# Kernel optimization log

Measured on AMD Instinct MI355X. Metric: run time of the kernel, lower is better.

The kernel has to match this reference:

```python
import jax, jax.numpy as jnp
import numpy as np

HEADS = 4
DIM_HEAD = 128


def setup_inputs() -> dict:
    key = jax.random.key(0)
    k1, k2, k3, k4 = jax.random.split(key, 4)
    B, C, H, W = 8, 256, 64, 64
    hidden = HEADS * DIM_HEAD  # 512
    x = jax.random.normal(k1, (B, C, H, W), dtype=jnp.float32)
    # 1x1 convs are just channel matmuls; store kernels as [out_ch, in_ch]
    w_qkv = jax.random.normal(k2, (3 * hidden, C), dtype=jnp.float32) * 0.05
    w_out = jax.random.normal(k3, (C, hidden), dtype=jnp.float32) * 0.05
    b_out = jax.random.normal(k4, (C,), dtype=jnp.float32) * 0.05
    return {"x": x, "w_qkv": w_qkv, "w_out": w_out, "b_out": b_out}


def reference(x, w_qkv, w_out, b_out):
    B, C, H, W = x.shape
    n = H * W
    # to_qkv: 1x1 conv without bias == channel matmul
    qkv = jnp.einsum('bchw,oc->bohw', x, w_qkv)  # [B, 3*heads*dim_head, H, W]
    qkv = qkv.reshape(B, 3, HEADS, DIM_HEAD, n)  # 'b (qkv heads c) h w -> b qkv heads c n'
    q, k, v = qkv[:, 0], qkv[:, 1], qkv[:, 2]    # each [B, heads, dim_head, n]
    k = jax.nn.softmax(k, axis=-1)               # softmax over spatial positions
    context = jnp.einsum('bhdn,bhen->bhde', k, v)   # [B, heads, d, e]
    out = jnp.einsum('bhde,bhdn->bhen', context, q)  # [B, heads, e, n]
    out = out.reshape(B, HEADS * DIM_HEAD, H, W)
    # to_out: 1x1 conv with bias
    return jnp.einsum('bchw,oc->bohw', out, w_out) + b_out[None, :, None, None]
```

## Files before the change

kernel.cpp:

```cpp
#include <hip/hip_runtime.h>
#include <stdint.h>


using frag8 = __attribute__((ext_vector_type(8))) short;
using f32x4 = __attribute__((ext_vector_type(4))) float;

__device__ __forceinline__ float bf2f(unsigned short u) {
    union { unsigned int u; float f; } c;
    c.u = ((unsigned int)u) << 16;
    return c.f;
}
__device__ __forceinline__ unsigned short f2bf(float f) {
    union { float f; unsigned int u; } c; c.f = f;
    unsigned int u = c.u;
    return (unsigned short)((u + 0x7FFFu + ((u >> 16) & 1u)) >> 16);
}

__device__ __forceinline__ void gl_lds16(const void* g, void* l) {
    __builtin_amdgcn_global_load_lds(
        (const __attribute__((address_space(1))) unsigned int*)g,
        (__attribute__((address_space(3))) unsigned int*)l, 16, 0, 0);
}

__global__ __launch_bounds__(256) void k0_weights(
    const float* __restrict__ w_qkv, const float* __restrict__ w_out,
    unsigned short* __restrict__ wkb, unsigned short* __restrict__ wqT,
    unsigned short* __restrict__ U, float* __restrict__ rs)
{
    __shared__ float T[64][65];
    const int blk = blockIdx.x;
    const int tid = threadIdx.x;
    if (blk < 128) {
        const int idx = (blk * 256 + tid) * 4;
        float4 v = *(const float4*)(w_qkv + 512 * 256 + idx);
        ushort4 o;
        o.x = f2bf(v.x); o.y = f2bf(v.y); o.z = f2bf(v.z); o.w = f2bf(v.w);
        *(ushort4*)(wkb + idx) = o;
    } else if (blk < 160) {
        const int t = blk - 128;
        const int j0 = (t >> 2) * 64, c0 = (t & 3) * 64;
        const int r = tid >> 4, cc = (tid & 15) * 4;
        #pragma unroll
        for (int p = 0; p < 4; ++p) {
            float4 v = *(const float4*)(w_qkv + (j0 + r + p * 16) * 256 + c0 + cc);
            T[r + p * 16][cc + 0] = v.x; T[r + p * 16][cc + 1] = v.y;
            T[r + p * 16][cc + 2] = v.z; T[r + p * 16][cc + 3] = v.w;
        }
        __syncthreads();
        const int c = tid >> 2, jj = (tid & 3) * 16;
        #pragma unroll
        for (int g = 0; g < 4; ++g) {
            ushort4 o;
            o.x = f2bf(T[jj + g * 4 + 0][c]);
            o.y = f2bf(T[jj + g * 4 + 1][c]);
            o.z = f2bf(T[jj + g * 4 + 2][c]);
            o.w = f2bf(T[jj + g * 4 + 3][c]);
            *(ushort4*)(wqT + (c0 + c) * 512 + j0 + jj + g * 4) = o;
        }
    } else if (blk < 224) {
        float (*As)[65] = &T[0];
        float (*Bs)[65] = &T[16];
        const int ub = blk - 160;
        const int h = ub >> 4, rem = ub & 15;
        const int o0 = (rem >> 2) * 64, c0 = (rem & 3) * 64;
        const int tm = tid >> 4, tn = tid & 15;
        const int ar = tid >> 2, ac = (tid & 3) * 4;
        const int br = tid >> 4, bc = (tid & 15) * 4;
        float acc[4][4] = {};
        for (int e0 = 0; e0 < 128; e0 += 16) {
            float4 a4 = *(const float4*)(w_out + (o0 + ar) * 512 + h * 128 + e0 + ac);
            float4 b4 = *(const float4*)(w_qkv + (1024 + h * 128 + e0 + br) * 256 + c0 + bc);
            __syncthreads();
            As[ac + 0][ar] = a4.x; As[ac + 1][ar] = a4.y;
            As[ac + 2][ar] = a4.z; As[ac + 3][ar] = a4.w;
            Bs[br][bc + 0] = b4.x; Bs[br][bc + 1] = b4.y;
            Bs[br][bc + 2] = b4.z; Bs[br][bc + 3] = b4.w;
            __syncthreads();
            #pragma unroll
            for (int kk = 0; kk < 16; ++kk) {
                float a[4], bb[4];
                #pragma unroll
                for (int i = 0; i < 4; ++i) a[i] = As[kk][tm * 4 + i];
                #pragma unroll
                for (int j = 0; j < 4; ++j) bb[j] = Bs[kk][tn * 4 + j];
                #pragma unroll
                for (int i = 0; i < 4; ++i)
                    #pragma unroll
                    for (int j = 0; j < 4; ++j) acc[i][j] += a[i] * bb[j];
            }
        }
        #pragma unroll
        for (int i = 0; i < 4; ++i) {
            ushort4 o;
            o.x = f2bf(acc[i][0]); o.y = f2bf(acc[i][1]);
            o.z = f2bf(acc[i][2]); o.w = f2bf(acc[i][3]);
            *(ushort4*)(U + h * 65536 + (o0 + tm * 4 + i) * 256 + c0 + tn * 4) = o;
        }
    } else {
        const int idx = ((blk - 224) * 256 + tid) * 4;
        *(float4*)(rs + idx) = make_float4(0.f, 0.f, 0.f, 0.f);
    }
}

__global__ __launch_bounds__(256) void k0_xt(
    const float* __restrict__ x, unsigned short* __restrict__ xbT,
    unsigned short* __restrict__ xbc)
{
    __shared__ float T[64][65];
    const int tid = threadIdx.x;
    const int n0 = blockIdx.x * 64, c0 = blockIdx.y * 64, b = blockIdx.z;
    const float* xb = x + (size_t)b * 1048576;
    const int cr = tid >> 4, nc = (tid & 15) * 4;
    #pragma unroll
    for (int p = 0; p < 4; ++p) {
        float4 v = *(const float4*)(xb + (size_t)(c0 + cr + p * 16) * 4096 + n0 + nc);
        T[cr + p * 16][nc + 0] = v.x; T[cr + p * 16][nc + 1] = v.y;
        T[cr + p * 16][nc + 2] = v.z; T[cr + p * 16][nc + 3] = v.w;
        ushort4 o;
        o.x = f2bf(v.x); o.y = f2bf(v.y); o.z = f2bf(v.z); o.w = f2bf(v.w);
        *(ushort4*)(xbc + (size_t)b * 1048576 + (size_t)(c0 + cr + p * 16) * 4096 + n0 + nc) = o;
    }
    __syncthreads();
    const int n = tid >> 2, cc = (tid & 3) * 16;
    unsigned short* dst = xbT + (size_t)b * 1048576 + (size_t)(n0 + n) * 256 + c0 + cc;
    #pragma unroll
    for (int g = 0; g < 4; ++g) {
        ushort4 o;
        o.x = f2bf(T[cc + g * 4 + 0][n]);
        o.y = f2bf(T[cc + g * 4 + 1][n]);
        o.z = f2bf(T[cc + g * 4 + 2][n]);
        o.w = f2bf(T[cc + g * 4 + 3][n]);
        *(ushort4*)(dst + g * 4) = o;
    }
}

template<int MODE>
__global__ __launch_bounds__(256) void mfma_bt(
    const unsigned short* __restrict__ A0, int lda,
    const unsigned short* __restrict__ B0, int ldb,
    void* __restrict__ C0, int ldc,
    const float* __restrict__ bias, int Kp,
    unsigned long long sAz, unsigned long long sBz, unsigned long long sCz,
    float* __restrict__ aux)
{
    __shared__ unsigned short As[128 * 32];
    __shared__ unsigned short Bs[128 * 32];
    const int tid  = threadIdx.x;
    const int w    = tid >> 6, lane = tid & 63;
    const int quad = lane >> 4, l16 = lane & 15;
    const int wm = (w >> 1) * 64, wn = (w & 1) * 64;
    const int z = blockIdx.z;

    const unsigned short* A;
    const unsigned short* B;
    int ks, ke, m0, n0;
    if constexpr (MODE == 3) {
        m0 = blockIdx.y * 128; n0 = 0;
        ks = 0; ke = 256;
        A = A0 + (unsigned long long)(z & 3) * 65536ull + (unsigned long long)m0 * lda;
        B = B0 + (unsigned long long)(z >> 2) * 131072ull + (unsigned long long)(z & 3) * 32768ull;
    } else if constexpr (MODE == 4) {
        m0 = blockIdx.y * 128; n0 = (blockIdx.x & 1) * 128;
        ks = (blockIdx.x >> 1) * 1024; ke = ks + 1024;
        A = A0 + sAz * z + (unsigned long long)m0 * lda;
        B = B0 + sBz * z + (unsigned long long)n0 * ldb;
    } else {
        m0 = blockIdx.y * 128; n0 = blockIdx.x * 128;
        ks = 0; ke = Kp;
        A = A0 + sAz * z + (unsigned long long)m0 * lda;
        B = B0 + sBz * z + (unsigned long long)n0 * ldb;
    }

    const int cA0 = w * 128 + lane;
    const int cA1 = cA0 + 64;
    const unsigned short* gA0 = A + (unsigned long long)(cA0 >> 2) * lda + (cA0 & 3) * 8;
    const unsigned short* gA1 = A + (unsigned long long)(cA1 >> 2) * lda + (cA1 & 3) * 8;
    const unsigned short* gB0 = B + (unsigned long long)(cA0 >> 2) * ldb + (cA0 & 3) * 8;
    const unsigned short* gB1 = B + (unsigned long long)(cA1 >> 2) * ldb + (cA1 & 3) * 8;
    unsigned short* lA0 = As + w * 1024;
    unsigned short* lA1 = As + w * 1024 + 512;
    unsigned short* lB0 = Bs + w * 1024;
    unsigned short* lB1 = Bs + w * 1024 + 512;

    f32x4 acc[4][4] = {};

    for (int k0 = ks; k0 < ke; k0 += 32) {
        gl_lds16(gA0 + k0, lA0);
        gl_lds16(gA1 + k0, lA1);
        gl_lds16(gB0 + k0, lB0);
        gl_lds16(gB1 + k0, lB1);
        __syncthreads();
        frag8 a[4], b[4];
        #pragma unroll
        for (int t = 0; t < 4; ++t) {
            a[t] = *(const frag8*)(As + (wm + t * 16 + l16) * 32 + quad * 8);
            b[t] = *(const frag8*)(Bs + (wn + t * 16 + l16) * 32 + quad * 8);
        }
        #pragma unroll
        for (int mt = 0; mt < 4; ++mt)
            #pragma unroll
            for (int nt = 0; nt < 4; ++nt)
                acc[mt][nt] = __builtin_amdgcn_mfma_f32_16x16x32_bf16(
                    a[mt], b[nt], acc[mt][nt], 0, 0, 0);
        __syncthreads();
    }

    if constexpr (MODE == 0 || MODE == 3) {
        unsigned short* C;
        if constexpr (MODE == 0)
            C = (unsigned short*)C0 + sCz * z + (unsigned long long)m0 * ldc + n0;
        else
            C = (unsigned short*)C0 + (unsigned long long)(z >> 2) * 131072ull
              + (unsigned long long)(z & 3) * 128ull + (unsigned long long)m0 * ldc;
        #pragma unroll
        for (int mt = 0; mt < 4; ++mt) {
            const int row = wm + mt * 16 + quad * 4;
            #pragma unroll
            for (int nt = 0; nt < 4; ++nt) {
                const int col = wn + nt * 16 + l16;
                #pragma unroll
                for (int r = 0; r < 4; ++r)
                    C[(unsigned long long)(row + r) * ldc + col] = f2bf(acc[mt][nt][r]);
            }
        }
    } else if constexpr (MODE == 1) {
        float* C = (float*)C0 + sCz * z + (unsigned long long)m0 * ldc + n0;
        const float* bp = bias + m0;
        #pragma unroll
        for (int mt = 0; mt < 4; ++mt) {
            const int row = wm + mt * 16 + quad * 4;
            #pragma unroll
            for (int nt = 0; nt < 4; ++nt) {
                const int col = wn + nt * 16 + l16;
                #pragma unroll
                for (int r = 0; r < 4; ++r)
                    C[(unsigned long long)(row + r) * ldc + col] = acc[mt][nt][r] + bp[row + r];
            }
        }
    } else if constexpr (MODE == 4) {
        float* C = (float*)C0 + (unsigned long long)(blockIdx.x >> 1) * 1048576ull
                 + sCz * z + (unsigned long long)m0 * ldc + n0;
        #pragma unroll
        for (int mt = 0; mt < 4; ++mt) {
            const int row = wm + mt * 16 + quad * 4;
            #pragma unroll
            for (int nt = 0; nt < 4; ++nt) {
                const int col = wn + nt * 16 + l16;
                #pragma unroll
                for (int r = 0; r < 4; ++r)
                    C[(unsigned long long)(row + r) * ldc + col] = acc[mt][nt][r];
            }
        }
    } else {
        unsigned short* C = (unsigned short*)C0 + sCz * z
                          + (unsigned long long)m0 * ldc + n0;
        float rp[4][4] = {};
        #pragma unroll
        for (int mt = 0; mt < 4; ++mt) {
            const int row = wm + mt * 16 + quad * 4;
            #pragma unroll
            for (int nt = 0; nt < 4; ++nt) {
                const int col = wn + nt * 16 + l16;
                #pragma unroll
                for (int r = 0; r < 4; ++r) {
                    const float e = __expf(acc[mt][nt][r]);
                    C[(unsigned long long)(row + r) * ldc + col] = f2bf(e);
                    rp[mt][r] += e;
                }
            }
        }
        #pragma unroll
        for (int m = 1; m < 16; m <<= 1)
            #pragma unroll
            for (int mt = 0; mt < 4; ++mt)
                #pragma unroll
                for (int r = 0; r < 4; ++r)
                    rp[mt][r] += __shfl_xor(rp[mt][r], m, 64);
        if (l16 == 0) {
            float* rsb = aux + z * 512 + m0;
            #pragma unroll
            for (int mt = 0; mt < 4; ++mt)
                #pragma unroll
                for (int r = 0; r < 4; ++r)
                    atomicAdd(rsb + wm + mt * 16 + quad * 4 + r, rp[mt][r]);
        }
    }
}

__global__ __launch_bounds__(256) void k3_sum(
    const float* __restrict__ Gp, const float* __restrict__ rs,
    unsigned short* __restrict__ G)
{
    const int idx = (blockIdx.x * 256 + threadIdx.x) * 4;
    const float inv = 1.0f / rs[idx >> 8];
    float4 s = make_float4(0.f, 0.f, 0.f, 0.f);
    #pragma unroll
    for (int sl = 0; sl < 4; ++sl) {
        float4 t = *(const float4*)(Gp + (size_t)sl * 1048576 + idx);
        s.x += t.x; s.y += t.y; s.z += t.z; s.w += t.w;
    }
    ushort4 o;
    o.x = f2bf(s.x * inv); o.y = f2bf(s.y * inv);
    o.z = f2bf(s.z * inv); o.w = f2bf(s.w * inv);
    *(ushort4*)(G + idx) = o;
}

extern "C" void kernel_launch(void* const* d_in, const int* in_sizes, int n_in,
                              void* d_out, int out_size, void* d_ws, size_t ws_size,
                              hipStream_t stream) {
    (void)in_sizes; (void)n_in; (void)out_size; (void)ws_size;
    const float* x     = (const float*)d_in[0];
    const float* w_qkv = (const float*)d_in[1];
    const float* w_out = (const float*)d_in[2];
    const float* b_out = (const float*)d_in[3];
    float* out = (float*)d_out;

    char* ws = (char*)d_ws;
    unsigned short* Kexp = (unsigned short*)ws;
    unsigned short* xbT  = (unsigned short*)(ws + 33554432);
    unsigned short* xbc  = (unsigned short*)(ws + 50331648);
    unsigned short* wkb  = (unsigned short*)(ws + 67108864);
    unsigned short* wqT  = (unsigned short*)(ws + 67371008);
    unsigned short* U    = (unsigned short*)(ws + 67633152);
    float*          rs   = (float*)(ws + 68157440);
    float*          Gp   = (float*)(ws + 68173824);
    unsigned short* G    = (unsigned short*)(ws + 84951040);
    unsigned short* Mb   = (unsigned short*)(ws + 87048192);
    unsigned short* Nb   = (unsigned short*)(ws + 89145344);

    k0_weights<<<dim3(228), 256, 0, stream>>>(w_qkv, w_out, wkb, wqT, U, rs);
    k0_xt<<<dim3(64, 4, 8), 256, 0, stream>>>(x, xbT, xbc);
    mfma_bt<5><<<dim3(32, 4, 8), 256, 0, stream>>>(
        wkb, 256, xbT, 256, Kexp, 4096, nullptr, 256,
        0ull, 1048576ull, 2097152ull, rs);
    mfma_bt<4><<<dim3(8, 4, 8), 256, 0, stream>>>(
        Kexp, 4096, xbc, 4096, Gp, 256, nullptr, 0,
        2097152ull, 1048576ull, 131072ull, nullptr);
    k3_sum<<<dim3(1024), 256, 0, stream>>>(Gp, rs, G);
    mfma_bt<3><<<dim3(1, 2, 32), 256, 0, stream>>>(
        U, 256, G, 256, Mb, 512, nullptr, 256,
        0ull, 0ull, 0ull, nullptr);
    mfma_bt<0><<<dim3(2, 2, 8), 256, 0, stream>>>(
        Mb, 512, wqT, 512, Nb, 256, nullptr, 512,
        131072ull, 0ull, 65536ull, nullptr);
    mfma_bt<1><<<dim3(32, 2, 8), 256, 0, stream>>>(
        Nb, 256, xbT, 256, out, 4096, b_out, 256,
        65536ull, 1048576ull, 1048576ull, nullptr);
}
```

Baseline: 201.5 us.

## Merge prep kernels, widen GEMM K-step, stage epilogue through LDS

```diff
diff --git a/kernel.cpp b/kernel.cpp
--- a/kernel.cpp
+++ b/kernel.cpp
@@ -4,6 +4,7 @@
 
 using frag8 = __attribute__((ext_vector_type(8))) short;
 using f32x4 = __attribute__((ext_vector_type(4))) float;
+typedef unsigned short us8 __attribute__((ext_vector_type(8)));
 
 __device__ __forceinline__ float bf2f(unsigned short u) {
     union { unsigned int u; float f; } c;
@@ -22,115 +23,126 @@
         (__attribute__((address_space(3))) unsigned int*)l, 16, 0, 0);
 }
 
-__global__ __launch_bounds__(256) void k0_weights(
-    const float* __restrict__ w_qkv, const float* __restrict__ w_out,
+__global__ __launch_bounds__(256) void k0_all(
+    const float* __restrict__ x, const float* __restrict__ w_qkv,
+    const float* __restrict__ w_out,
+    unsigned short* __restrict__ xbT, unsigned short* __restrict__ xbc,
     unsigned short* __restrict__ wkb, unsigned short* __restrict__ wqT,
     unsigned short* __restrict__ U, float* __restrict__ rs)
 {
-    __shared__ float T[64][65];
+    __shared__ __align__(16) unsigned char sm[68096];
     const int blk = blockIdx.x;
     const int tid = threadIdx.x;
-    if (blk < 128) {
-        const int idx = (blk * 256 + tid) * 4;
-        float4 v = *(const float4*)(w_qkv + 512 * 256 + idx);
-        ushort4 o;
-        o.x = f2bf(v.x); o.y = f2bf(v.y); o.z = f2bf(v.z); o.w = f2bf(v.w);
-        *(ushort4*)(wkb + idx) = o;
-    } else if (blk < 160) {
-        const int t = blk - 128;
-        const int j0 = (t >> 2) * 64, c0 = (t & 3) * 64;
-        const int r = tid >> 4, cc = (tid & 15) * 4;
-        #pragma unroll
-        for (int p = 0; p < 4; ++p) {
-            float4 v = *(const float4*)(w_qkv + (j0 + r + p * 16) * 256 + c0 + cc);
-            T[r + p * 16][cc + 0] = v.x; T[r + p * 16][cc + 1] = v.y;
-            T[r + p * 16][cc + 2] = v.z; T[r + p * 16][cc + 3] = v.w;
+    if (blk < 512) {
+        float (*T)[133] = (float(*)[133])sm;
+        const int b = blk >> 6, rem = blk & 63;
+        const int n0 = (rem >> 1) * 128, c0 = (rem & 1) * 128;
+        const float* xb = x + (size_t)b * 1048576;
+        const int rr = tid >> 5, cc4 = (tid & 31) * 4;
+        #pragma unroll
+        for (int p = 0; p < 16; ++p) {
+            const int r = rr + p * 8;
+            float4 v = *(const float4*)(xb + (size_t)(c0 + r) * 4096 + n0 + cc4);
+            T[r][cc4 + 0] = v.x; T[r][cc4 + 1] = v.y;
+            T[r][cc4 + 2] = v.z; T[r][cc4 + 3] = v.w;
         }
         __syncthreads();
-        const int c = tid >> 2, jj = (tid & 3) * 16;
-        #pragma unroll
-        for (int g = 0; g < 4; ++g) {
+        const int nr = tid >> 4, c8 = (tid & 15) * 8;
+        unsigned short* dst = xbT + (size_t)b * 1048576 + (size_t)n0 * 256 + c0;
+        #pragma unroll
+        for (int p = 0; p < 8; ++p) {
+            const int n = nr + p * 16;
+            us8 o;
+            #pragma unroll
+            for (int j = 0; j < 8; ++j) o[j] = f2bf(T[c8 + j][n]);
+            *(us8*)(dst + (size_t)n * 256 + c8) = o;
+        }
+    } else if (blk < 1024) {
+        const int base = (blk - 512) * 16384;
+        #pragma unroll
+        for (int p = 0; p < 8; ++p) {
+            const int idx = base + p * 2048 + tid * 8;
+            float4 a = *(const float4*)(x + idx);
+            float4 b = *(const float4*)(x + idx + 4);
+            us8 o;
+            o[0] = f2bf(a.x); o[1] = f2bf(a.y); o[2] = f2bf(a.z); o[3] = f2bf(a.w);
+            o[4] = f2bf(b.x); o[5] = f2bf(b.y); o[6] = f2bf(b.z); o[7] = f2bf(b.w);
+            *(us8*)(xbc + idx) = o;
+        }
+    } else {
+        const int wb = blk - 1024;
+        if (wb < 128) {
+            const int idx = (wb * 256 + tid) * 4;
+            float4 v = *(const float4*)(w_qkv + 512 * 256 + idx);
             ushort4 o;
-            o.x = f2bf(T[jj + g * 4 + 0][c]);
-            o.y = f2bf(T[jj + g * 4 + 1][c]);
-            o.z = f2bf(T[jj + g * 4 + 2][c]);
-            o.w = f2bf(T[jj + g * 4 + 3][c]);
-            *(ushort4*)(wqT + (c0 + c) * 512 + j0 + jj + g * 4) = o;
-        }
-    } else if (blk < 224) {
-        float (*As)[65] = &T[0];
-        float (*Bs)[65] = &T[16];
-        const int ub = blk - 160;
-        const int h = ub >> 4, rem = ub & 15;
-        const int o0 = (rem >> 2) * 64, c0 = (rem & 3) * 64;
-        const int tm = tid >> 4, tn = tid & 15;
-        const int ar = tid >> 2, ac = (tid & 3) * 4;
-        const int br = tid >> 4, bc = (tid & 15) * 4;
-        float acc[4][4] = {};
-        for (int e0 = 0; e0 < 128; e0 += 16) {
-            float4 a4 = *(const float4*)(w_out + (o0 + ar) * 512 + h * 128 + e0 + ac);
-            float4 b4 = *(const float4*)(w_qkv + (1024 + h * 128 + e0 + br) * 256 + c0 + bc);
+            o.x = f2bf(v.x); o.y = f2bf(v.y); o.z = f2bf(v.z); o.w = f2bf(v.w);
+            *(ushort4*)(wkb + idx) = o;
+        } else if (wb < 160) {
+            float (*T)[65] = (float(*)[65])sm;
+            const int t = wb - 128;
+            const int j0 = (t >> 2) * 64, c0 = (t & 3) * 64;
+            const int r = tid >> 4, cc = (tid & 15) * 4;
+            #pragma unroll
+            for (int p = 0; p < 4; ++p) {
+                float4 v = *(const float4*)(w_qkv + (j0 + r + p * 16) * 256 + c0 + cc);
+                T[r + p * 16][cc + 0] = v.x; T[r + p * 16][cc + 1] = v.y;
+                T[r + p * 16][cc + 2] = v.z; T[r + p * 16][cc + 3] = v.w;
+            }
             __syncthreads();
-            As[ac + 0][ar] = a4.x; As[ac + 1][ar] = a4.y;
-            As[ac + 2][ar] = a4.z; As[ac + 3][ar] = a4.w;
-            Bs[br][bc + 0] = b4.x; Bs[br][bc + 1] = b4.y;
-            Bs[br][bc + 2] = b4.z; Bs[br][bc + 3] = b4.w;
-            __syncthreads();
-            #pragma unroll
-            for (int kk = 0; kk < 16; ++kk) {
-                float a[4], bb[4];
-                #pragma unroll
-                for (int i = 0; i < 4; ++i) a[i] = As[kk][tm * 4 + i];
-                #pragma unroll
-                for (int j = 0; j < 4; ++j) bb[j] = Bs[kk][tn * 4 + j];
-                #pragma unroll
-                for (int i = 0; i < 4; ++i)
+            const int c = tid >> 2, jj = (tid & 3) * 16;
+            #pragma unroll
+            for (int g = 0; g < 4; ++g) {
+                ushort4 o;
+                o.x = f2bf(T[jj + g * 4 + 0][c]);
+                o.y = f2bf(T[jj + g * 4 + 1][c]);
+                o.z = f2bf(T[jj + g * 4 + 2][c]);
+                o.w = f2bf(T[jj + g * 4 + 3][c]);
+                *(ushort4*)(wqT + (c0 + c) * 512 + j0 + jj + g * 4) = o;
+            }
+        } else if (wb < 224) {
+            float (*T)[65] = (float(*)[65])sm;
+            float (*As)[65] = &T[0];
+            float (*Bs)[65] = &T[16];
+            const int ub = wb - 160;
+            const int h = ub >> 4, rem = ub & 15;
+            const int o0 = (rem >> 2) * 64, c0 = (rem & 3) * 64;
+            const int tm = tid >> 4, tn = tid & 15;
+            const int ar = tid >> 2, ac = (tid & 3) * 4;
+            const int br = tid >> 4, bc = (tid & 15) * 4;
+            float acc[4][4] = {};
+            for (int e0 = 0; e0 < 128; e0 += 16) {
+                float4 a4 = *(const float4*)(w_out + (o0 + ar) * 512 + h * 128 + e0 + ac);
+                float4 b4 = *(const float4*)(w_qkv + (1024 + h * 128 + e0 + br) * 256 + c0 + bc);
+                __syncthreads();
+                As[ac + 0][ar] = a4.x; As[ac + 1][ar] = a4.y;
+                As[ac + 2][ar] = a4.z; As[ac + 3][ar] = a4.w;
+                Bs[br][bc + 0] = b4.x; Bs[br][bc + 1] = b4.y;
+                Bs[br][bc + 2] = b4.z; Bs[br][bc + 3] = b4.w;
+                __syncthreads();
+                #pragma unroll
+                for (int kk = 0; kk < 16; ++kk) {
+                    float a[4], bb[4];
                     #pragma unroll
-                    for (int j = 0; j < 4; ++j) acc[i][j] += a[i] * bb[j];
-            }
-        }
-        #pragma unroll
-        for (int i = 0; i < 4; ++i) {
-            ushort4 o;
-            o.x = f2bf(acc[i][0]); o.y = f2bf(acc[i][1]);
-            o.z = f2bf(acc[i][2]); o.w = f2bf(acc[i][3]);
-            *(ushort4*)(U + h * 65536 + (o0 + tm * 4 + i) * 256 + c0 + tn * 4) = o;
-        }
-    } else {
-        const int idx = ((blk - 224) * 256 + tid) * 4;
-        *(float4*)(rs + idx) = make_float4(0.f, 0.f, 0.f, 0.f);
-    }
-}
-
-__global__ __launch_bounds__(256) void k0_xt(
-    const float* __restrict__ x, unsigned short* __restrict__ xbT,
-    unsigned short* __restrict__ xbc)
-{
-    __shared__ float T[64][65];
-    const int tid = threadIdx.x;
-    const int n0 = blockIdx.x * 64, c0 = blockIdx.y * 64, b = blockIdx.z;
-    const float* xb = x + (size_t)b * 1048576;
-    const int cr = tid >> 4, nc = (tid & 15) * 4;
-    #pragma unroll
-    for (int p = 0; p < 4; ++p) {
-        float4 v = *(const float4*)(xb + (size_t)(c0 + cr + p * 16) * 4096 + n0 + nc);
-        T[cr + p * 16][nc + 0] = v.x; T[cr + p * 16][nc + 1] = v.y;
-        T[cr + p * 16][nc + 2] = v.z; T[cr + p * 16][nc + 3] = v.w;
-        ushort4 o;
-        o.x = f2bf(v.x); o.y = f2bf(v.y); o.z = f2bf(v.z); o.w = f2bf(v.w);
-        *(ushort4*)(xbc + (size_t)b * 1048576 + (size_t)(c0 + cr + p * 16) * 4096 + n0 + nc) = o;
-    }
-    __syncthreads();
-    const int n = tid >> 2, cc = (tid & 3) * 16;
-    unsigned short* dst = xbT + (size_t)b * 1048576 + (size_t)(n0 + n) * 256 + c0 + cc;
-    #pragma unroll
-    for (int g = 0; g < 4; ++g) {
-        ushort4 o;
-        o.x = f2bf(T[cc + g * 4 + 0][n]);
-        o.y = f2bf(T[cc + g * 4 + 1][n]);
-        o.z = f2bf(T[cc + g * 4 + 2][n]);
-        o.w = f2bf(T[cc + g * 4 + 3][n]);
-        *(ushort4*)(dst + g * 4) = o;
+                    for (int i = 0; i < 4; ++i) a[i] = As[kk][tm * 4 + i];
+                    #pragma unroll
+                    for (int j = 0; j < 4; ++j) bb[j] = Bs[kk][tn * 4 + j];
+                    #pragma unroll
+                    for (int i = 0; i < 4; ++i)
+                        #pragma unroll
+                        for (int j = 0; j < 4; ++j) acc[i][j] += a[i] * bb[j];
+                }
+            }
+            #pragma unroll
+            for (int i = 0; i < 4; ++i) {
+                ushort4 o;
+                o.x = f2bf(acc[i][0]); o.y = f2bf(acc[i][1]);
+                o.z = f2bf(acc[i][2]); o.w = f2bf(acc[i][3]);
+                *(ushort4*)(U + h * 65536 + (o0 + tm * 4 + i) * 256 + c0 + tn * 4) = o;
+            }
+        } else {
+            const int idx = ((wb - 224) * 256 + tid) * 4;
+            *(float4*)(rs + idx) = make_float4(0.f, 0.f, 0.f, 0.f);
+        }
     }
 }
 
@@ -143,8 +155,11 @@
     unsigned long long sAz, unsigned long long sBz, unsigned long long sCz,
     float* __restrict__ aux)
 {
-    __shared__ unsigned short As[128 * 32];
-    __shared__ unsigned short Bs[128 * 32];
+    __shared__ __align__(16) unsigned char smem[67584];
+    unsigned short* As = (unsigned short*)smem;
+    unsigned short* Bs = (unsigned short*)(smem + 16384);
+    float (*CS)[132] = (float(*)[132])smem;
+
     const int tid  = threadIdx.x;
     const int w    = tid >> 6, lane = tid & 63;
     const int quad = lane >> 4, l16 = lane & 15;
@@ -171,47 +186,47 @@
         B = B0 + sBz * z + (unsigned long long)n0 * ldb;
     }
 
-    const int cA0 = w * 128 + lane;
-    const int cA1 = cA0 + 64;
-    const unsigned short* gA0 = A + (unsigned long long)(cA0 >> 2) * lda + (cA0 & 3) * 8;
-    const unsigned short* gA1 = A + (unsigned long long)(cA1 >> 2) * lda + (cA1 & 3) * 8;
-    const unsigned short* gB0 = B + (unsigned long long)(cA0 >> 2) * ldb + (cA0 & 3) * 8;
-    const unsigned short* gB1 = B + (unsigned long long)(cA1 >> 2) * ldb + (cA1 & 3) * 8;
-    unsigned short* lA0 = As + w * 1024;
-    unsigned short* lA1 = As + w * 1024 + 512;
-    unsigned short* lB0 = Bs + w * 1024;
-    unsigned short* lB1 = Bs + w * 1024 + 512;
+    const unsigned short* gA[4];
+    const unsigned short* gB[4];
+    int lo[4];
+    #pragma unroll
+    for (int i = 0; i < 4; ++i) {
+        const int q = i * 256 + w * 64 + lane;
+        const int s = q >> 9, r = (q >> 2) & 127, ko = (q & 3) * 8 + s * 32;
+        gA[i] = A + (unsigned long long)r * lda + ko;
+        gB[i] = B + (unsigned long long)r * ldb + ko;
+        lo[i] = q * 8;
+    }
 
     f32x4 acc[4][4] = {};
 
-    for (int k0 = ks; k0 < ke; k0 += 32) {
-        gl_lds16(gA0 + k0, lA0);
-        gl_lds16(gA1 + k0, lA1);
-        gl_lds16(gB0 + k0, lB0);
-        gl_lds16(gB1 + k0, lB1);
+    for (int k0 = ks; k0 < ke; k0 += 64) {
+        #pragma unroll
+        for (int i = 0; i < 4; ++i) {
+            gl_lds16(gA[i] + k0, As + lo[i]);
+            gl_lds16(gB[i] + k0, Bs + lo[i]);
+        }
         __syncthreads();
-        frag8 a[4], b[4];
-        #pragma unroll
-        for (int t = 0; t < 4; ++t) {
-            a[t] = *(const frag8*)(As + (wm + t * 16 + l16) * 32 + quad * 8);
-            b[t] = *(const frag8*)(Bs + (wn + t * 16 + l16) * 32 + quad * 8);
-        }
-        #pragma unroll
-        for (int mt = 0; mt < 4; ++mt)
-            #pragma unroll
-            for (int nt = 0; nt < 4; ++nt)
-                acc[mt][nt] = __builtin_amdgcn_mfma_f32_16x16x32_bf16(
-                    a[mt], b[nt], acc[mt][nt], 0, 0, 0);
+        #pragma unroll
+        for (int s = 0; s < 2; ++s) {
+            frag8 a[4], b[4];
+            #pragma unroll
+            for (int t = 0; t < 4; ++t) {
+                a[t] = *(const frag8*)(As + s * 4096 + (wm + t * 16 + l16) * 32 + quad * 8);
+                b[t] = *(const frag8*)(Bs + s * 4096 + (wn + t * 16 + l16) * 32 + quad * 8);
+            }
+            #pragma unroll
+            for (int mt = 0; mt < 4; ++mt)
+                #pragma unroll
+                for (int nt = 0; nt < 4; ++nt)
+                    acc[mt][nt] = __builtin_amdgcn_mfma_f32_16x16x32_bf16(
+                        a[mt], b[nt], acc[mt][nt], 0, 0, 0);
+        }
         __syncthreads();
     }
 
-    if constexpr (MODE == 0 || MODE == 3) {
-        unsigned short* C;
-        if constexpr (MODE == 0)
-            C = (unsigned short*)C0 + sCz * z + (unsigned long long)m0 * ldc + n0;
-        else
-            C = (unsigned short*)C0 + (unsigned long long)(z >> 2) * 131072ull
-              + (unsigned long long)(z & 3) * 128ull + (unsigned long long)m0 * ldc;
+    if constexpr (MODE == 5) {
+        float rp[4][4] = {};
         #pragma unroll
         for (int mt = 0; mt < 4; ++mt) {
             const int row = wm + mt * 16 + quad * 4;
@@ -219,52 +234,9 @@
             for (int nt = 0; nt < 4; ++nt) {
                 const int col = wn + nt * 16 + l16;
                 #pragma unroll
-                for (int r = 0; r < 4; ++r)
-                    C[(unsigned long long)(row + r) * ldc + col] = f2bf(acc[mt][nt][r]);
-            }
-        }
-    } else if constexpr (MODE == 1) {
-        float* C = (float*)C0 + sCz * z + (unsigned long long)m0 * ldc + n0;
-        const float* bp = bias + m0;
-        #pragma unroll
-        for (int mt = 0; mt < 4; ++mt) {
-            const int row = wm + mt * 16 + quad * 4;
-            #pragma unroll
-            for (int nt = 0; nt < 4; ++nt) {
-                const int col = wn + nt * 16 + l16;
-                #pragma unroll
-                for (int r = 0; r < 4; ++r)
-                    C[(unsigned long long)(row + r) * ldc + col] = acc[mt][nt][r] + bp[row + r];
-            }
-        }
-    } else if constexpr (MODE == 4) {
-        float* C = (float*)C0 + (unsigned long long)(blockIdx.x >> 1) * 1048576ull
-                 + sCz * z + (unsigned long long)m0 * ldc + n0;
-        #pragma unroll
-        for (int mt = 0; mt < 4; ++mt) {
-            const int row = wm + mt * 16 + quad * 4;
-            #pragma unroll
-            for (int nt = 0; nt < 4; ++nt) {
-                const int col = wn + nt * 16 + l16;
-                #pragma unroll
-                for (int r = 0; r < 4; ++r)
-                    C[(unsigned long long)(row + r) * ldc + col] = acc[mt][nt][r];
-            }
-        }
-    } else {
-        unsigned short* C = (unsigned short*)C0 + sCz * z
-                          + (unsigned long long)m0 * ldc + n0;
-        float rp[4][4] = {};
-        #pragma unroll
-        for (int mt = 0; mt < 4; ++mt) {
-            const int row = wm + mt * 16 + quad * 4;
-            #pragma unroll
-            for (int nt = 0; nt < 4; ++nt) {
-                const int col = wn + nt * 16 + l16;
-                #pragma unroll
                 for (int r = 0; r < 4; ++r) {
                     const float e = __expf(acc[mt][nt][r]);
-                    C[(unsigned long long)(row + r) * ldc + col] = f2bf(e);
+                    CS[row + r][col] = e;
                     rp[mt][r] += e;
                 }
             }
@@ -283,6 +255,55 @@
                 #pragma unroll
                 for (int r = 0; r < 4; ++r)
                     atomicAdd(rsb + wm + mt * 16 + quad * 4 + r, rp[mt][r]);
+        }
+    } else {
+        #pragma unroll
+        for (int mt = 0; mt < 4; ++mt) {
+            const int row = wm + mt * 16 + quad * 4;
+            #pragma unroll
+            for (int nt = 0; nt < 4; ++nt) {
+                const int col = wn + nt * 16 + l16;
+                #pragma unroll
+                for (int r = 0; r < 4; ++r)
+                    CS[row + r][col] = acc[mt][nt][r];
+            }
+        }
+    }
+    __syncthreads();
+
+    if constexpr (MODE == 1 || MODE == 4) {
+        float* C;
+        if constexpr (MODE == 1)
+            C = (float*)C0 + sCz * z + (unsigned long long)m0 * ldc + n0;
+        else
+            C = (float*)C0 + (unsigned long long)(blockIdx.x >> 1) * 1048576ull
+              + sCz * z + (unsigned long long)m0 * ldc + n0;
+        const int lr0 = tid >> 5, c4 = (tid & 31) * 4;
+        #pragma unroll
+        for (int p = 0; p < 16; ++p) {
+            const int lr = lr0 + p * 8;
+            float4 v = *(const float4*)&CS[lr][c4];
+            if constexpr (MODE == 1) {
+                const float bv = bias[m0 + lr];
+                v.x += bv; v.y += bv; v.z += bv; v.w += bv;
+            }
+            *(float4*)(C + (unsigned long long)lr * ldc + c4) = v;
+        }
+    } else {
+        unsigned short* C;
+        if constexpr (MODE == 3)
+            C = (unsigned short*)C0 + (unsigned long long)(z >> 2) * 131072ull
+              + (unsigned long long)(z & 3) * 128ull + (unsigned long long)m0 * ldc;
+        else
+            C = (unsigned short*)C0 + sCz * z + (unsigned long long)m0 * ldc + n0;
+        const int lr0 = tid >> 4, c8 = (tid & 15) * 8;
+        #pragma unroll
+        for (int p = 0; p < 8; ++p) {
+            const int lr = lr0 + p * 16;
+            us8 o;
+            #pragma unroll
+            for (int j = 0; j < 8; ++j) o[j] = f2bf(CS[lr][c8 + j]);
+            *(us8*)(C + (unsigned long long)lr * ldc + c8) = o;
         }
     }
 }
@@ -328,8 +349,7 @@
     unsigned short* Mb   = (unsigned short*)(ws + 87048192);
     unsigned short* Nb   = (unsigned short*)(ws + 89145344);
 
-    k0_weights<<<dim3(228), 256, 0, stream>>>(w_qkv, w_out, wkb, wqT, U, rs);
-    k0_xt<<<dim3(64, 4, 8), 256, 0, stream>>>(x, xbT, xbc);
+    k0_all<<<dim3(1252), 256, 0, stream>>>(x, w_qkv, w_out, xbT, xbc, wkb, wqT, U, rs);
     mfma_bt<5><<<dim3(32, 4, 8), 256, 0, stream>>>(
         wkb, 256, xbT, 256, Kexp, 4096, nullptr, 256,
         0ull, 1048576ull, 2097152ull, rs);
```

Measured after the change: 198.2 us. Within noise of the previous version (-1.7%).
